# Kernel optimization log

Measured on AMD Instinct MI355X. Metric: run time of the kernel, lower is better.

The kernel has to match this reference:

```python
import jax, jax.numpy as jnp
import numpy as np

C = 256
CI = C // 2  # inter_channel = 128
B, H, W = 8, 64, 64


def setup_inputs() -> dict:
    key = jax.random.key(0)
    ks = jax.random.split(key, 9)
    s = 0.02
    return {
        "x": jax.random.normal(ks[0], (B, C, H, W), jnp.float32),
        "w_phi": jax.random.normal(ks[1], (CI, C), jnp.float32) * s,
        "b_phi": jax.random.normal(ks[2], (CI,), jnp.float32) * s,
        "w_theta": jax.random.normal(ks[3], (CI, C), jnp.float32) * s,
        "b_theta": jax.random.normal(ks[4], (CI,), jnp.float32) * s,
        "w_g": jax.random.normal(ks[5], (CI, C), jnp.float32) * s,
        "b_g": jax.random.normal(ks[6], (CI,), jnp.float32) * s,
        "w_mask": jax.random.normal(ks[7], (C, CI), jnp.float32) * s,
        "b_mask": jax.random.normal(ks[8], (C,), jnp.float32) * s,
    }


def reference(x, w_phi, b_phi, w_theta, b_theta, w_g, b_g, w_mask, b_mask):
    b, c, h, w = x.shape
    n = h * w
    xf = x.reshape(b, c, n)  # [b, c, n]
    # 1x1 convs == per-position channel projections
    phi = jnp.einsum('dc,bcn->bdn', w_phi, xf) + b_phi[:, None]      # [b, ci, n]
    theta = jnp.einsum('dc,bcn->bnd', w_theta, xf) + b_theta[None, None, :]  # [b, n, ci]
    g = jnp.einsum('dc,bcn->bnd', w_g, xf) + b_g[None, None, :]      # [b, n, ci]
    # full self-attention over spatial positions (no scaling, as in source)
    scores = jnp.einsum('bnd,bdm->bnm', theta, phi)                  # [b, n, n]
    attn = jax.nn.softmax(scores, axis=-1)
    y = jnp.einsum('bnm,bmd->bnd', attn, g)                          # [b, n, ci]
    # mask conv (1x1) back to channel dim + residual
    mask = jnp.einsum('cd,bnd->bcn', w_mask, y) + b_mask[:, None]    # [b, c, n]
    return mask.reshape(b, c, h, w) + x
```

## Files before the change

kernel.cpp:

```cpp
#include <hip/hip_runtime.h>

#define BB 8
#define CC 256
#define DD 128
#define NN 4096

#define LOG2E 1.44269504f
#define MSHIFT 32.0f

typedef __attribute__((ext_vector_type(8))) short short8;
typedef __attribute__((ext_vector_type(4))) short short4v;
typedef __attribute__((ext_vector_type(4))) float f32x4;
typedef __attribute__((ext_vector_type(16))) float f32x16;
typedef __attribute__((ext_vector_type(4))) unsigned int u32x4;

static __device__ __forceinline__ unsigned short f2bf(float f) {
    unsigned u = __builtin_bit_cast(unsigned, f);
    u += 0x7FFFu + ((u >> 16) & 1u);
    return (unsigned short)(u >> 16);
}
static __device__ __forceinline__ float bf2f(unsigned short h) {
    unsigned u = ((unsigned)h) << 16;
    return __builtin_bit_cast(float, u);
}
static __device__ __forceinline__ short8 pack8(float4 a, float4 b) {
    short8 r;
    r[0] = (short)f2bf(a.x); r[1] = (short)f2bf(a.y);
    r[2] = (short)f2bf(a.z); r[3] = (short)f2bf(a.w);
    r[4] = (short)f2bf(b.x); r[5] = (short)f2bf(b.y);
    r[6] = (short)f2bf(b.z); r[7] = (short)f2bf(b.w);
    return r;
}
static __device__ __forceinline__ unsigned cvtpk_bf16(float lo, float hi) {
    unsigned r;
    asm("v_cvt_pk_bf16_f32 %0, %1, %2" : "=v"(r) : "v"(lo), "v"(hi));
    return r;
}
static __device__ __forceinline__ void pl32swap(unsigned &a, unsigned &b) {
#if __has_builtin(__builtin_amdgcn_permlane32_swap)
    auto r = __builtin_amdgcn_permlane32_swap((int)a, (int)b, false, false);
    a = (unsigned)r[0]; b = (unsigned)r[1];
#else
    asm("v_permlane32_swap_b32 %0, %1" : "+v"(a), "+v"(b));
#endif
}

__global__ __launch_bounds__(256) void k_proj(
        const float* __restrict__ x,
        const float* __restrict__ w_phi, const float* __restrict__ b_phi,
        const float* __restrict__ w_theta, const float* __restrict__ b_theta,
        const float* __restrict__ w_g, const float* __restrict__ b_g,
        unsigned short* __restrict__ qws, unsigned short* __restrict__ kws,
        unsigned short* __restrict__ vtws) {
    __shared__ __align__(16) unsigned short xs[128][72];
    __shared__ __align__(16) unsigned short rp[128][136];
    int nb = blockIdx.x * 128, proj = blockIdx.y, b = blockIdx.z;
    const float *W, *bias;
    if (proj == 0) { W = w_theta; bias = b_theta; }
    else if (proj == 1) { W = w_phi; bias = b_phi; }
    else { W = w_g; bias = b_g; }
    float scl = (proj == 0) ? LOG2E : 1.0f;
    int t = threadIdx.x, lane = t & 63, wave = t >> 6;
    int l16 = lane & 15, l4 = lane >> 4;

    f32x4 acc[2][8];
#pragma unroll
    for (int mf = 0; mf < 2; mf++)
#pragma unroll
        for (int nf = 0; nf < 8; nf++)
#pragma unroll
            for (int e = 0; e < 4; e++) acc[mf][nf][e] = 0.f;

    const float* xpb = x + (size_t)b * CC * NN;
    int cl = t >> 2;
    int gq = t & 3;
    int n0 = gq * 32;
    int wcol = (cl + 16 * gq) & 63;

    for (int kc = 0; kc < 4; kc++) {
        int c0k = kc * 64;
        __syncthreads();
        {
            const float* src = xpb + (size_t)(c0k + cl) * NN + nb + n0;
            float4 xv[8];
#pragma unroll
            for (int j = 0; j < 8; j++) xv[j] = *(const float4*)(src + 4 * j);
#pragma unroll
            for (int j = 0; j < 8; j++) {
                xs[n0 + 4 * j + 0][wcol] = f2bf(xv[j].x);
                xs[n0 + 4 * j + 1][wcol] = f2bf(xv[j].y);
                xs[n0 + 4 * j + 2][wcol] = f2bf(xv[j].z);
                xs[n0 + 4 * j + 3][wcol] = f2bf(xv[j].w);
            }
        }
        __syncthreads();
        short8 af[2][2];
#pragma unroll
        for (int mf = 0; mf < 2; mf++)
#pragma unroll
            for (int ic = 0; ic < 2; ic++) {
                int d = wave * 32 + mf * 16 + l16;
                const float* wp = W + d * CC + c0k + ic * 32 + l4 * 8;
                af[mf][ic] = pack8(*(const float4*)wp, *(const float4*)(wp + 4));
            }
#pragma unroll
        for (int nf = 0; nf < 8; nf++)
#pragma unroll
            for (int ic = 0; ic < 2; ic++) {
                int rcol = (ic * 32 + l4 * 8 + 16 * (nf >> 1)) & 63;
                short8 bfr = *(const short8*)&xs[nf * 16 + l16][rcol];
                acc[0][nf] = __builtin_amdgcn_mfma_f32_16x16x32_bf16(af[0][ic], bfr, acc[0][nf], 0, 0, 0);
                acc[1][nf] = __builtin_amdgcn_mfma_f32_16x16x32_bf16(af[1][ic], bfr, acc[1][nf], 0, 0, 0);
            }
    }
    __syncthreads();
    if (proj < 2) {
        unsigned short* outp = (proj == 0 ? qws : kws) + (size_t)b * NN * DD;
#pragma unroll
        for (int mf = 0; mf < 2; mf++) {
            int d0 = wave * 32 + mf * 16 + l4 * 4;
            float bb[4];
#pragma unroll
            for (int r = 0; r < 4; r++) bb[r] = bias[d0 + r];
#pragma unroll
            for (int nf = 0; nf < 8; nf++) {
                short4v pk;
#pragma unroll
                for (int r = 0; r < 4; r++) pk[r] = (short)f2bf((acc[mf][nf][r] + bb[r]) * scl);
                *(short4v*)&rp[nf * 16 + l16][d0] = pk;
            }
        }
        __syncthreads();
#pragma unroll
        for (int i = 0; i < 8; i++) {
            int idx = t + 256 * i;
            int n = idx >> 4, dd = (idx & 15) * 8;
            *(short8*)(outp + (size_t)(nb + n) * DD + dd) = *(const short8*)&rp[n][dd];
        }
    } else {
#pragma unroll
        for (int mf = 0; mf < 2; mf++) {
            int drow = wave * 32 + mf * 16 + l4 * 4;
            float bb[4];
#pragma unroll
            for (int r = 0; r < 4; r++) bb[r] = bias[drow + r];
#pragma unroll
            for (int nf = 0; nf < 8; nf++)
#pragma unroll
                for (int r = 0; r < 4; r++)
                    rp[drow + r][nf * 16 + l16] = f2bf(acc[mf][nf][r] + bb[r]);
        }
        __syncthreads();
        unsigned short* outp = vtws + (size_t)b * DD * NN;
#pragma unroll
        for (int i = 0; i < 8; i++) {
            int idx = t + 256 * i;
            int d = idx >> 4, n0s = (idx & 15) * 8;
            *(short8*)(outp + (size_t)d * NN + nb + n0s) = *(const short8*)&rp[d][n0s];
        }
    }
}

__global__ __launch_bounds__(128, 2) void k_flash(
        const unsigned short* __restrict__ q, const unsigned short* __restrict__ kk,
        const unsigned short* __restrict__ vt, unsigned short* __restrict__ opart,
        float* __restrict__ lsums) {
    __shared__ __align__(16) unsigned char smem[32768];

    int bid = blockIdx.x;
    int b   = bid & 7;
    int rem = bid >> 3;
    int ks  = rem >> 6;
    int qt  = rem & 63;
    int qb  = qt * 64;

    int t = threadIdx.x, lane = t & 63, wave = t >> 6;
    int l31 = lane & 31, hi = lane >> 5;

    const unsigned short* qp = q  + (size_t)b * NN * DD;
    const unsigned short* kp = kk + (size_t)b * NN * DD;
    const unsigned short* vp = vt + (size_t)b * DD * NN;

    short8 qreg[8];
    {
        int qrow = qb + wave * 32 + l31;
#pragma unroll
        for (int kc = 0; kc < 8; kc++)
            qreg[kc] = *(const short8*)(qp + (size_t)qrow * DD + kc * 16 + hi * 8);
    }

    f32x16 o[4];
#pragma unroll
    for (int df = 0; df < 4; df++)
#pragma unroll
        for (int e = 0; e < 16; e++) o[df][e] = 0.f;
    float lsum0 = 0.f, lsum1 = 0.f;

    int kbase = ks * (NN / 2);
    const int NIT = (NN / 2) / 32;

    {
        uint4 k0[4], v0[4];
#pragma unroll
        for (int i = 0; i < 4; i++) {
            int idx = t + 128 * i;
            k0[i] = *(const uint4*)(kp + (size_t)(kbase + (idx >> 4)) * DD + (idx & 15) * 8);
            v0[i] = *(const uint4*)(vp + (size_t)(idx >> 2) * NN + kbase + (idx & 3) * 8);
        }
#pragma unroll
        for (int i = 0; i < 4; i++) {
            int idx = t + 128 * i;
            int rk = idx >> 4, ck = idx & 15;
            *(uint4*)((char*)smem + rk * 256 + ((ck ^ (rk & 7)) << 4)) = k0[i];
            int rv = idx >> 2, cv = idx & 3;
            *(uint4*)((char*)smem + 16384 + rv * 64 + ((cv ^ ((rv ^ (rv >> 2)) & 3)) << 4)) = v0[i];
        }
    }
    __syncthreads();

    for (int it = 0; it < NIT; ++it) {
        char* Kb  = (char*)smem + (it & 1) * 8192;
        char* Vb  = (char*)smem + 16384 + (it & 1) * 8192;
        char* Kb2 = (char*)smem + ((it & 1) ^ 1) * 8192;
        char* Vb2 = (char*)smem + 16384 + (((it & 1) ^ 1)) * 8192;

        uint4 kreg[4], vreg[4];
        bool pf = (it + 1 < NIT);
        if (pf) {
            int mb2 = kbase + (it + 1) * 32;
#pragma unroll
            for (int i = 0; i < 4; i++) {
                int idx = t + 128 * i;
                kreg[i] = *(const uint4*)(kp + (size_t)(mb2 + (idx >> 4)) * DD + (idx & 15) * 8);
                vreg[i] = *(const uint4*)(vp + (size_t)(idx >> 2) * NN + mb2 + (idx & 3) * 8);
            }
        }

        f32x16 sA, sB;
#pragma unroll
        for (int e = 0; e < 16; e++) { sA[e] = -MSHIFT; sB[e] = 0.f; }
        __builtin_amdgcn_s_setprio(1);
#pragma unroll
        for (int kc = 0; kc < 8; kc += 2) {
            short8 a0 = *(const short8*)(Kb + l31 * 256 + ((((kc << 1) | hi) ^ (l31 & 7)) << 4));
            short8 a1 = *(const short8*)(Kb + l31 * 256 + (((((kc + 1) << 1) | hi) ^ (l31 & 7)) << 4));
            sA = __builtin_amdgcn_mfma_f32_32x32x16_bf16(a0, qreg[kc], sA, 0, 0, 0);
            sB = __builtin_amdgcn_mfma_f32_32x32x16_bf16(a1, qreg[kc + 1], sB, 0, 0, 0);
        }
        __builtin_amdgcn_s_setprio(0);

        u32x4 pa[2];
        {
            float p[16];
#pragma unroll
            for (int r = 0; r < 16; r++) {
                p[r] = __builtin_exp2f(sA[r] + sB[r]);
                if (r & 1) lsum1 += p[r]; else lsum0 += p[r];
            }
#pragma unroll
            for (int h = 0; h < 2; h++) {
                unsigned a0 = cvtpk_bf16(p[8 * h + 0], p[8 * h + 1]);
                unsigned a1 = cvtpk_bf16(p[8 * h + 2], p[8 * h + 3]);
                unsigned b0 = cvtpk_bf16(p[8 * h + 4], p[8 * h + 5]);
                unsigned b1 = cvtpk_bf16(p[8 * h + 6], p[8 * h + 7]);
                pl32swap(a0, b0);
                pl32swap(a1, b1);
                u32x4 v; v[0] = a0; v[1] = a1; v[2] = b0; v[3] = b1;
                pa[h] = v;
            }
        }

        __builtin_amdgcn_s_setprio(1);
#pragma unroll
        for (int df = 0; df < 4; df++) {
            int row = df * 32 + l31;
            int sw = (row ^ (row >> 2)) & 3;
#pragma unroll
            for (int c = 0; c < 2; c++) {
                short8 vb = *(const short8*)(Vb + row * 64 + ((((c << 1) | hi) ^ sw) << 4));
                o[df] = __builtin_amdgcn_mfma_f32_32x32x16_bf16(
                    __builtin_bit_cast(short8, pa[c]), vb, o[df], 0, 0, 0);
            }
        }
        __builtin_amdgcn_s_setprio(0);

        if (pf) {
#pragma unroll
            for (int i = 0; i < 4; i++) {
                int idx = t + 128 * i;
                int rk = idx >> 4, ck = idx & 15;
                *(uint4*)(Kb2 + rk * 256 + ((ck ^ (rk & 7)) << 4)) = kreg[i];
                int rv = idx >> 2, cv = idx & 3;
                *(uint4*)(Vb2 + rv * 64 + ((cv ^ ((rv ^ (rv >> 2)) & 3)) << 4)) = vreg[i];
            }
        }
        __syncthreads();
    }

    {
        float lsum = lsum0 + lsum1;
        float tot = lsum + __shfl_xor(lsum, 32);
        if (lane < 32)
            lsums[((size_t)ks * BB + b) * NN + qb + wave * 32 + l31] = tot;
    }
    unsigned short (*Ox)[136] = (unsigned short (*)[136])smem;
#pragma unroll
    for (int df = 0; df < 4; df++)
#pragma unroll
        for (int r = 0; r < 16; r++) {
            int qr = (r & 3) + 8 * (r >> 2) + 4 * hi;
            Ox[wave * 32 + qr][df * 32 + l31] = f2bf(o[df][r]);
        }
    __syncthreads();
    unsigned short* op = opart + (((size_t)ks * BB + b) * NN + qb) * DD;
#pragma unroll
    for (int i = 0; i < 8; i++) {
        int idx = t + 128 * i;
        int nr = idx >> 4, c0 = (idx & 15) * 8;
        *(short8*)(op + (size_t)nr * DD + c0) = *(const short8*)&Ox[nr][c0];
    }
}

__global__ __launch_bounds__(256) void k_maskout(
        const unsigned short* __restrict__ opart, const float* __restrict__ lsums,
        const float* __restrict__ w_mask, const float* __restrict__ b_mask,
        const float* __restrict__ x, float* __restrict__ out) {
    __shared__ __align__(16) unsigned char pool[35072];
    unsigned short (*Ys)[136] = (unsigned short (*)[136])pool;
    float (*Os)[68] = (float (*)[68])pool;
    float* invl = (float*)(pool + 34816);
    int nb = blockIdx.x * 64, cs = blockIdx.y, b = blockIdx.z;
    int t = threadIdx.x, lane = t & 63, wave = t >> 6;
    int l16 = lane & 15, l4 = lane >> 4;

    const unsigned short* o0 = opart + ((size_t)b * NN + nb) * DD;
    const unsigned short* o1 = opart + (((size_t)BB + b) * NN + nb) * DD;
    if (t < 64) {
        float ls0 = lsums[(size_t)b * NN + nb + t];
        float ls1 = lsums[((size_t)BB + b) * NN + nb + t];
        invl[t] = 1.0f / (ls0 + ls1);
    }
    __syncthreads();
#pragma unroll
    for (int i = 0; i < 4; i++) {
        int idx = t + 256 * i;
        int nr = idx >> 4, d0 = (idx & 15) * 8;
        short8 a = *(const short8*)(o0 + (size_t)nr * DD + d0);
        short8 c = *(const short8*)(o1 + (size_t)nr * DD + d0);
        float inv = invl[nr];
        short8 yv;
#pragma unroll
        for (int j = 0; j < 8; j++)
            yv[j] = (short)f2bf((bf2f((unsigned short)a[j]) + bf2f((unsigned short)c[j])) * inv);
        *(short8*)&Ys[nr][d0] = yv;
    }
    __syncthreads();

    f32x4 acc[2][4];
#pragma unroll
    for (int mf = 0; mf < 2; mf++)
#pragma unroll
        for (int nf = 0; nf < 4; nf++)
#pragma unroll
            for (int e = 0; e < 4; e++) acc[mf][nf][e] = 0.f;

#pragma unroll
    for (int kc = 0; kc < 4; kc++) {
        int d0 = kc * 32 + l4 * 8;
        short8 af[2];
#pragma unroll
        for (int mf = 0; mf < 2; mf++) {
            int c = cs * 128 + wave * 32 + mf * 16 + l16;
            const float* wp = w_mask + c * DD + d0;
            af[mf] = pack8(*(const float4*)wp, *(const float4*)(wp + 4));
        }
#pragma unroll
        for (int nf = 0; nf < 4; nf++) {
            short8 bfr = *(const short8*)&Ys[nf * 16 + l16][d0];
#pragma unroll
            for (int mf = 0; mf < 2; mf++)
                acc[mf][nf] = __builtin_amdgcn_mfma_f32_16x16x32_bf16(af[mf], bfr, acc[mf][nf], 0, 0, 0);
        }
    }
    __syncthreads();

#pragma unroll
    for (int mf = 0; mf < 2; mf++) {
        int c0 = wave * 32 + mf * 16 + l4 * 4;
        float bb[4];
#pragma unroll
        for (int r = 0; r < 4; r++) bb[r] = b_mask[cs * 128 + c0 + r];
#pragma unroll
        for (int r = 0; r < 4; r++)
#pragma unroll
            for (int nf = 0; nf < 4; nf++)
                Os[c0 + r][nf * 16 + l16] = acc[mf][nf][r] + bb[r];
    }
    __syncthreads();

    const float* xp = x + (size_t)b * CC * NN + (size_t)cs * 128 * NN + nb;
    float* op = out + (size_t)b * CC * NN + (size_t)cs * 128 * NN + nb;
#pragma unroll
    for (int i = 0; i < 8; i++) {
        int idx = t + 256 * i;
        int c = idx >> 4, nq = (idx & 15) * 4;
        float4 osv = *(const float4*)&Os[c][nq];
        float4 xv = *(const float4*)(xp + (size_t)c * NN + nq);
        float4 ov;
        ov.x = osv.x + xv.x; ov.y = osv.y + xv.y;
        ov.z = osv.z + xv.z; ov.w = osv.w + xv.w;
        *(float4*)(op + (size_t)c * NN + nq) = ov;
    }
}

extern "C" void kernel_launch(void* const* d_in, const int* in_sizes, int n_in,
                              void* d_out, int out_size, void* d_ws, size_t ws_size,
                              hipStream_t stream) {
    const float* x       = (const float*)d_in[0];
    const float* w_phi   = (const float*)d_in[1];
    const float* b_phi   = (const float*)d_in[2];
    const float* w_theta = (const float*)d_in[3];
    const float* b_theta = (const float*)d_in[4];
    const float* w_g     = (const float*)d_in[5];
    const float* b_g     = (const float*)d_in[6];
    const float* w_mask  = (const float*)d_in[7];
    const float* b_mask  = (const float*)d_in[8];
    float* out = (float*)d_out;

    char* ws = (char*)d_ws;
    unsigned short* opart = (unsigned short*)(ws);
    unsigned short* qw    = (unsigned short*)(ws + ((size_t)16 << 20));
    unsigned short* kw    = (unsigned short*)(ws + ((size_t)24 << 20));
    unsigned short* vtw   = (unsigned short*)(ws + ((size_t)32 << 20));
    float*          lsums = (float*)(ws + ((size_t)40 << 20));

    k_proj<<<dim3(NN / 128, 3, BB), 256, 0, stream>>>(x, w_phi, b_phi, w_theta, b_theta,
                                                      w_g, b_g, qw, kw, vtw);
    k_flash<<<dim3(1024, 1, 1), 128, 0, stream>>>(qw, kw, vtw, opart, lsums);
    k_maskout<<<dim3(NN / 64, 2, BB), 256, 0, stream>>>(opart, lsums, w_mask, b_mask, x, out);
}
```

Baseline: 233.4 us.

## Fuse three projections into one block and loop channel halves in maskout

The projection kernel now computes theta, phi and g in a single 512-thread block, so each x tile is loaded and converted to bf16 once instead of three times, with waves split across d and n. The mask-output kernel now handles both 128-channel halves in one block, so the partial-output combine and normalisation run once per tile instead of twice. The cost is more accumulator registers per thread, fewer blocks in flight, and more shared memory in maskout, which may lower occupancy.

New measurement: 238.3 us. +2.1%, slower.

```diff
diff --git a/kernel.cpp b/kernel.cpp
--- a/kernel.cpp
+++ b/kernel.cpp
@@ -45,7 +45,7 @@
 #endif
 }
 
-__global__ __launch_bounds__(256) void k_proj(
+__global__ __launch_bounds__(512, 2) void k_proj(
         const float* __restrict__ x,
         const float* __restrict__ w_phi, const float* __restrict__ b_phi,
         const float* __restrict__ w_theta, const float* __restrict__ b_theta,
@@ -54,107 +54,144 @@
         unsigned short* __restrict__ vtws) {
     __shared__ __align__(16) unsigned short xs[128][72];
     __shared__ __align__(16) unsigned short rp[128][136];
-    int nb = blockIdx.x * 128, proj = blockIdx.y, b = blockIdx.z;
-    const float *W, *bias;
-    if (proj == 0) { W = w_theta; bias = b_theta; }
-    else if (proj == 1) { W = w_phi; bias = b_phi; }
-    else { W = w_g; bias = b_g; }
-    float scl = (proj == 0) ? LOG2E : 1.0f;
+    int nb = blockIdx.x * 128, b = blockIdx.y;
     int t = threadIdx.x, lane = t & 63, wave = t >> 6;
     int l16 = lane & 15, l4 = lane >> 4;
-
-    f32x4 acc[2][8];
+    int wd = wave & 3, wn = wave >> 2;
+
+    f32x4 a_th[2][4], a_ph[2][4], a_g[2][4];
 #pragma unroll
     for (int mf = 0; mf < 2; mf++)
 #pragma unroll
-        for (int nf = 0; nf < 8; nf++)
-#pragma unroll
-            for (int e = 0; e < 4; e++) acc[mf][nf][e] = 0.f;
+        for (int nf = 0; nf < 4; nf++)
+#pragma unroll
+            for (int e = 0; e < 4; e++) { a_th[mf][nf][e] = 0.f; a_ph[mf][nf][e] = 0.f; a_g[mf][nf][e] = 0.f; }
 
     const float* xpb = x + (size_t)b * CC * NN;
-    int cl = t >> 2;
-    int gq = t & 3;
-    int n0 = gq * 32;
-    int wcol = (cl + 16 * gq) & 63;
 
     for (int kc = 0; kc < 4; kc++) {
         int c0k = kc * 64;
         __syncthreads();
         {
-            const float* src = xpb + (size_t)(c0k + cl) * NN + nb + n0;
-            float4 xv[8];
-#pragma unroll
-            for (int j = 0; j < 8; j++) xv[j] = *(const float4*)(src + 4 * j);
-#pragma unroll
-            for (int j = 0; j < 8; j++) {
-                xs[n0 + 4 * j + 0][wcol] = f2bf(xv[j].x);
-                xs[n0 + 4 * j + 1][wcol] = f2bf(xv[j].y);
-                xs[n0 + 4 * j + 2][wcol] = f2bf(xv[j].z);
-                xs[n0 + 4 * j + 3][wcol] = f2bf(xv[j].w);
+            float4 xv[4];
+#pragma unroll
+            for (int j = 0; j < 4; j++) {
+                int idx = t + 512 * j;
+                int cr = idx >> 5, pos = idx & 31;
+                xv[j] = *(const float4*)(xpb + (size_t)(c0k + cr) * NN + nb + pos * 4);
+            }
+#pragma unroll
+            for (int j = 0; j < 4; j++) {
+                int idx = t + 512 * j;
+                int cr = idx >> 5, pos = idx & 31;
+                int col = (cr + 8 * (pos >> 2)) & 63;
+                xs[pos * 4 + 0][col] = f2bf(xv[j].x);
+                xs[pos * 4 + 1][col] = f2bf(xv[j].y);
+                xs[pos * 4 + 2][col] = f2bf(xv[j].z);
+                xs[pos * 4 + 3][col] = f2bf(xv[j].w);
             }
         }
         __syncthreads();
-        short8 af[2][2];
+        short8 af_t[2][2], af_p[2][2], af_g[2][2];
 #pragma unroll
         for (int mf = 0; mf < 2; mf++)
 #pragma unroll
             for (int ic = 0; ic < 2; ic++) {
-                int d = wave * 32 + mf * 16 + l16;
-                const float* wp = W + d * CC + c0k + ic * 32 + l4 * 8;
-                af[mf][ic] = pack8(*(const float4*)wp, *(const float4*)(wp + 4));
-            }
-#pragma unroll
-        for (int nf = 0; nf < 8; nf++)
+                int d = wd * 32 + mf * 16 + l16;
+                int co = c0k + ic * 32 + l4 * 8;
+                const float* wpt = w_theta + d * CC + co;
+                const float* wpp = w_phi   + d * CC + co;
+                const float* wpg = w_g     + d * CC + co;
+                af_t[mf][ic] = pack8(*(const float4*)wpt, *(const float4*)(wpt + 4));
+                af_p[mf][ic] = pack8(*(const float4*)wpp, *(const float4*)(wpp + 4));
+                af_g[mf][ic] = pack8(*(const float4*)wpg, *(const float4*)(wpg + 4));
+            }
+#pragma unroll
+        for (int nf = 0; nf < 4; nf++)
 #pragma unroll
             for (int ic = 0; ic < 2; ic++) {
-                int rcol = (ic * 32 + l4 * 8 + 16 * (nf >> 1)) & 63;
-                short8 bfr = *(const short8*)&xs[nf * 16 + l16][rcol];
-                acc[0][nf] = __builtin_amdgcn_mfma_f32_16x16x32_bf16(af[0][ic], bfr, acc[0][nf], 0, 0, 0);
-                acc[1][nf] = __builtin_amdgcn_mfma_f32_16x16x32_bf16(af[1][ic], bfr, acc[1][nf], 0, 0, 0);
-            }
-    }
-    __syncthreads();
-    if (proj < 2) {
-        unsigned short* outp = (proj == 0 ? qws : kws) + (size_t)b * NN * DD;
-#pragma unroll
-        for (int mf = 0; mf < 2; mf++) {
-            int d0 = wave * 32 + mf * 16 + l4 * 4;
-            float bb[4];
-#pragma unroll
-            for (int r = 0; r < 4; r++) bb[r] = bias[d0 + r];
-#pragma unroll
-            for (int nf = 0; nf < 8; nf++) {
-                short4v pk;
-#pragma unroll
-                for (int r = 0; r < 4; r++) pk[r] = (short)f2bf((acc[mf][nf][r] + bb[r]) * scl);
-                *(short4v*)&rp[nf * 16 + l16][d0] = pk;
-            }
-        }
-        __syncthreads();
-#pragma unroll
-        for (int i = 0; i < 8; i++) {
-            int idx = t + 256 * i;
+                int ncol = (ic * 32 + l4 * 8 + 8 * (wn * 4 + nf)) & 63;
+                short8 bfr = *(const short8*)&xs[wn * 64 + nf * 16 + l16][ncol];
+                a_th[0][nf] = __builtin_amdgcn_mfma_f32_16x16x32_bf16(af_t[0][ic], bfr, a_th[0][nf], 0, 0, 0);
+                a_th[1][nf] = __builtin_amdgcn_mfma_f32_16x16x32_bf16(af_t[1][ic], bfr, a_th[1][nf], 0, 0, 0);
+                a_ph[0][nf] = __builtin_amdgcn_mfma_f32_16x16x32_bf16(af_p[0][ic], bfr, a_ph[0][nf], 0, 0, 0);
+                a_ph[1][nf] = __builtin_amdgcn_mfma_f32_16x16x32_bf16(af_p[1][ic], bfr, a_ph[1][nf], 0, 0, 0);
+                a_g[0][nf]  = __builtin_amdgcn_mfma_f32_16x16x32_bf16(af_g[0][ic], bfr, a_g[0][nf], 0, 0, 0);
+                a_g[1][nf]  = __builtin_amdgcn_mfma_f32_16x16x32_bf16(af_g[1][ic], bfr, a_g[1][nf], 0, 0, 0);
+            }
+    }
+    __syncthreads();
+
+#pragma unroll
+    for (int mf = 0; mf < 2; mf++) {
+        int d0 = wd * 32 + mf * 16 + l4 * 4;
+        float bb[4];
+#pragma unroll
+        for (int r = 0; r < 4; r++) bb[r] = b_theta[d0 + r];
+#pragma unroll
+        for (int nf = 0; nf < 4; nf++) {
+            short4v pk;
+#pragma unroll
+            for (int r = 0; r < 4; r++) pk[r] = (short)f2bf((a_th[mf][nf][r] + bb[r]) * LOG2E);
+            *(short4v*)&rp[wn * 64 + nf * 16 + l16][d0] = pk;
+        }
+    }
+    __syncthreads();
+    {
+        unsigned short* outp = qws + (size_t)b * NN * DD;
+#pragma unroll
+        for (int i = 0; i < 4; i++) {
+            int idx = t + 512 * i;
             int n = idx >> 4, dd = (idx & 15) * 8;
             *(short8*)(outp + (size_t)(nb + n) * DD + dd) = *(const short8*)&rp[n][dd];
         }
-    } else {
-#pragma unroll
-        for (int mf = 0; mf < 2; mf++) {
-            int drow = wave * 32 + mf * 16 + l4 * 4;
-            float bb[4];
-#pragma unroll
-            for (int r = 0; r < 4; r++) bb[r] = bias[drow + r];
-#pragma unroll
-            for (int nf = 0; nf < 8; nf++)
-#pragma unroll
-                for (int r = 0; r < 4; r++)
-                    rp[drow + r][nf * 16 + l16] = f2bf(acc[mf][nf][r] + bb[r]);
-        }
-        __syncthreads();
+    }
+    __syncthreads();
+
+#pragma unroll
+    for (int mf = 0; mf < 2; mf++) {
+        int d0 = wd * 32 + mf * 16 + l4 * 4;
+        float bb[4];
+#pragma unroll
+        for (int r = 0; r < 4; r++) bb[r] = b_phi[d0 + r];
+#pragma unroll
+        for (int nf = 0; nf < 4; nf++) {
+            short4v pk;
+#pragma unroll
+            for (int r = 0; r < 4; r++) pk[r] = (short)f2bf(a_ph[mf][nf][r] + bb[r]);
+            *(short4v*)&rp[wn * 64 + nf * 16 + l16][d0] = pk;
+        }
+    }
+    __syncthreads();
+    {
+        unsigned short* outp = kws + (size_t)b * NN * DD;
+#pragma unroll
+        for (int i = 0; i < 4; i++) {
+            int idx = t + 512 * i;
+            int n = idx >> 4, dd = (idx & 15) * 8;
+            *(short8*)(outp + (size_t)(nb + n) * DD + dd) = *(const short8*)&rp[n][dd];
+        }
+    }
+    __syncthreads();
+
+#pragma unroll
+    for (int mf = 0; mf < 2; mf++) {
+        int drow = wd * 32 + mf * 16 + l4 * 4;
+        float bb[4];
+#pragma unroll
+        for (int r = 0; r < 4; r++) bb[r] = b_g[drow + r];
+#pragma unroll
+        for (int nf = 0; nf < 4; nf++)
+#pragma unroll
+            for (int r = 0; r < 4; r++)
+                rp[drow + r][wn * 64 + nf * 16 + l16] = f2bf(a_g[mf][nf][r] + bb[r]);
+    }
+    __syncthreads();
+    {
         unsigned short* outp = vtws + (size_t)b * DD * NN;
 #pragma unroll
-        for (int i = 0; i < 8; i++) {
-            int idx = t + 256 * i;
+        for (int i = 0; i < 4; i++) {
+            int idx = t + 512 * i;
             int d = idx >> 4, n0s = (idx & 15) * 8;
             *(short8*)(outp + (size_t)d * NN + nb + n0s) = *(const short8*)&rp[d][n0s];
         }
@@ -325,11 +362,11 @@
         const unsigned short* __restrict__ opart, const float* __restrict__ lsums,
         const float* __restrict__ w_mask, const float* __restrict__ b_mask,
         const float* __restrict__ x, float* __restrict__ out) {
-    __shared__ __align__(16) unsigned char pool[35072];
+    __shared__ __align__(16) unsigned char pool[52480];
     unsigned short (*Ys)[136] = (unsigned short (*)[136])pool;
-    float (*Os)[68] = (float (*)[68])pool;
-    float* invl = (float*)(pool + 34816);
-    int nb = blockIdx.x * 64, cs = blockIdx.y, b = blockIdx.z;
+    float (*Os)[68] = (float (*)[68])(pool + 17408);
+    float* invl = (float*)(pool + 52224);
+    int nb = blockIdx.x * 64, b = blockIdx.y;
     int t = threadIdx.x, lane = t & 63, wave = t >> 6;
     int l16 = lane & 15, l4 = lane >> 4;
 
@@ -356,60 +393,62 @@
     }
     __syncthreads();
 
-    f32x4 acc[2][4];
-#pragma unroll
-    for (int mf = 0; mf < 2; mf++)
-#pragma unroll
-        for (int nf = 0; nf < 4; nf++)
-#pragma unroll
-            for (int e = 0; e < 4; e++) acc[mf][nf][e] = 0.f;
-
-#pragma unroll
-    for (int kc = 0; kc < 4; kc++) {
-        int d0 = kc * 32 + l4 * 8;
-        short8 af[2];
+    for (int cs = 0; cs < 2; cs++) {
+        f32x4 acc[2][4];
+#pragma unroll
+        for (int mf = 0; mf < 2; mf++)
+#pragma unroll
+            for (int nf = 0; nf < 4; nf++)
+#pragma unroll
+                for (int e = 0; e < 4; e++) acc[mf][nf][e] = 0.f;
+
+#pragma unroll
+        for (int kc = 0; kc < 4; kc++) {
+            int d0 = kc * 32 + l4 * 8;
+            short8 af[2];
+#pragma unroll
+            for (int mf = 0; mf < 2; mf++) {
+                int c = cs * 128 + wave * 32 + mf * 16 + l16;
+                const float* wp = w_mask + c * DD + d0;
+                af[mf] = pack8(*(const float4*)wp, *(const float4*)(wp + 4));
+            }
+#pragma unroll
+            for (int nf = 0; nf < 4; nf++) {
+                short8 bfr = *(const short8*)&Ys[nf * 16 + l16][d0];
+#pragma unroll
+                for (int mf = 0; mf < 2; mf++)
+                    acc[mf][nf] = __builtin_amdgcn_mfma_f32_16x16x32_bf16(af[mf], bfr, acc[mf][nf], 0, 0, 0);
+            }
+        }
+        __syncthreads();
+
 #pragma unroll
         for (int mf = 0; mf < 2; mf++) {
-            int c = cs * 128 + wave * 32 + mf * 16 + l16;
-            const float* wp = w_mask + c * DD + d0;
-            af[mf] = pack8(*(const float4*)wp, *(const float4*)(wp + 4));
-        }
-#pragma unroll
-        for (int nf = 0; nf < 4; nf++) {
-            short8 bfr = *(const short8*)&Ys[nf * 16 + l16][d0];
-#pragma unroll
-            for (int mf = 0; mf < 2; mf++)
-                acc[mf][nf] = __builtin_amdgcn_mfma_f32_16x16x32_bf16(af[mf], bfr, acc[mf][nf], 0, 0, 0);
-        }
-    }
-    __syncthreads();
-
-#pragma unroll
-    for (int mf = 0; mf < 2; mf++) {
-        int c0 = wave * 32 + mf * 16 + l4 * 4;
-        float bb[4];
-#pragma unroll
-        for (int r = 0; r < 4; r++) bb[r] = b_mask[cs * 128 + c0 + r];
-#pragma unroll
-        for (int r = 0; r < 4; r++)
-#pragma unroll
-            for (int nf = 0; nf < 4; nf++)
-                Os[c0 + r][nf * 16 + l16] = acc[mf][nf][r] + bb[r];
-    }
-    __syncthreads();
-
-    const float* xp = x + (size_t)b * CC * NN + (size_t)cs * 128 * NN + nb;
-    float* op = out + (size_t)b * CC * NN + (size_t)cs * 128 * NN + nb;
-#pragma unroll
-    for (int i = 0; i < 8; i++) {
-        int idx = t + 256 * i;
-        int c = idx >> 4, nq = (idx & 15) * 4;
-        float4 osv = *(const float4*)&Os[c][nq];
-        float4 xv = *(const float4*)(xp + (size_t)c * NN + nq);
-        float4 ov;
-        ov.x = osv.x + xv.x; ov.y = osv.y + xv.y;
-        ov.z = osv.z + xv.z; ov.w = osv.w + xv.w;
-        *(float4*)(op + (size_t)c * NN + nq) = ov;
+            int c0 = wave * 32 + mf * 16 + l4 * 4;
+            float bb[4];
+#pragma unroll
+            for (int r = 0; r < 4; r++) bb[r] = b_mask[cs * 128 + c0 + r];
+#pragma unroll
+            for (int r = 0; r < 4; r++)
+#pragma unroll
+                for (int nf = 0; nf < 4; nf++)
+                    Os[c0 + r][nf * 16 + l16] = acc[mf][nf][r] + bb[r];
+        }
+        __syncthreads();
+
+        const float* xp = x + (size_t)b * CC * NN + (size_t)cs * 128 * NN + nb;
+        float* op = out + (size_t)b * CC * NN + (size_t)cs * 128 * NN + nb;
+#pragma unroll
+        for (int i = 0; i < 8; i++) {
+            int idx = t + 256 * i;
+            int c = idx >> 4, nq = (idx & 15) * 4;
+            float4 osv = *(const float4*)&Os[c][nq];
+            float4 xv = *(const float4*)(xp + (size_t)c * NN + nq);
+            float4 ov;
+            ov.x = osv.x + xv.x; ov.y = osv.y + xv.y;
+            ov.z = osv.z + xv.z; ov.w = osv.w + xv.w;
+            *(float4*)(op + (size_t)c * NN + nq) = ov;
+        }
     }
 }
 
@@ -434,8 +473,8 @@
     unsigned short* vtw   = (unsigned short*)(ws + ((size_t)32 << 20));
     float*          lsums = (float*)(ws + ((size_t)40 << 20));
 
-    k_proj<<<dim3(NN / 128, 3, BB), 256, 0, stream>>>(x, w_phi, b_phi, w_theta, b_theta,
-                                                      w_g, b_g, qw, kw, vtw);
+    k_proj<<<dim3(NN / 128, BB), 512, 0, stream>>>(x, w_phi, b_phi, w_theta, b_theta,
+                                                   w_g, b_g, qw, kw, vtw);
     k_flash<<<dim3(1024, 1, 1), 128, 0, stream>>>(qw, kw, vtw, opart, lsums);
-    k_maskout<<<dim3(NN / 64, 2, BB), 256, 0, stream>>>(opart, lsums, w_mask, b_mask, x, out);
-}
+    k_maskout<<<dim3(NN / 64, BB), 256, 0, stream>>>(opart, lsums, w_mask, b_mask, x, out);
+}
```
